# Kernel optimization log

Measured on AMD Instinct MI355X. Metric: run time of the kernel, lower is better.

## Reference

```python
import jax, jax.numpy as jnp
import numpy as np

INIT_STDEV = 0.01

def setup_inputs() -> dict:
    key = jax.random.key(0)
    k1, k2, k3 = jax.random.split(key, 3)
    B, S, D = 8, 4096, 768
    x = jax.random.normal(k1, (B, S, D), dtype=jnp.float32)
    att_v = jax.random.normal(k2, (D,), dtype=jnp.float32) * INIT_STDEV
    att_W = jax.random.normal(k3, (D, D), dtype=jnp.float32) * INIT_STDEV
    return {"x": x, "att_v": att_v, "att_W": att_W}

def reference(x, att_v, att_W):
    # y = x @ W : [B,S,D]; scores = tanh(y) . v over D : [B,S]
    y = jnp.tanh(jnp.einsum('bsd,de->bse', x, att_W))
    scores = jnp.einsum('bsd,d->bs', y, att_v)
    weights = jax.nn.softmax(scores, axis=-1)            # softmax over sequence
    out = jnp.einsum('bs,bsd->bd', weights, x)           # attsum pool
    return out.astype(jnp.float32)
```

## Files before the change

### kernel.cpp

```cpp
#include <hip/hip_runtime.h>
#include <hip/hip_bf16.h>

constexpr int Bb = 8;
constexpr int Ss = 4096;
constexpr int Dd = 768;
constexpr int Mm = Bb * Ss;

typedef __bf16 bf16x8 __attribute__((ext_vector_type(8)));
typedef __bf16 bf16x4 __attribute__((ext_vector_type(4)));
typedef float f32x4 __attribute__((ext_vector_type(4)));

__device__ __forceinline__ float fast_tanh(float x) {
    return 1.f - 2.f / (__expf(2.f * x) + 1.f);
}

__device__ __forceinline__ void load_lds16(const void* g, void* l) {
    __builtin_amdgcn_global_load_lds(
        (const __attribute__((address_space(1))) unsigned int*)g,
        (__attribute__((address_space(3))) unsigned int*)l, 16, 0, 0);
}

__global__ __launch_bounds__(256) void convW(const float* __restrict__ W,
                                             __bf16* __restrict__ Wt) {
    __shared__ float tile[32][33];
    const int tx = threadIdx.x & 31;
    const int ty = threadIdx.x >> 5;
    const int kb = blockIdx.x * 32;
    const int nb = blockIdx.y * 32;
#pragma unroll
    for (int i = 0; i < 32; i += 8)
        tile[ty + i][tx] = W[(size_t)(kb + ty + i) * Dd + nb + tx];
    __syncthreads();
#pragma unroll
    for (int i = 0; i < 32; i += 8) {
        const int n = nb + ty + i;
        const int txs = (tx & 7) | ((((tx >> 3) & 3) ^ ((n >> 1) & 3)) << 3);
        Wt[(size_t)n * Dd + kb + txs] = (__bf16)tile[tx][ty + i];
    }
}

__global__ __launch_bounds__(512, 4) void scores_gemm(
    const float* __restrict__ x, const __bf16* __restrict__ Wt,
    const float* __restrict__ v, float* __restrict__ scores3) {
    __shared__ __bf16 As[3][128 * 32];
    __shared__ __bf16 Bs[3][256 * 32];
    __shared__ float ssc[8][64];

    const int t = threadIdx.x;
    const int id = blockIdx.x;
    const int ids = ((id & 7) * 96) + (id >> 3);
    const int mb = ids / 3;
    const int nb = ids - mb * 3;
    const int lane = t & 63;
    const int wave = t >> 6;
    const int wm = wave >> 2;
    const int wn = wave & 3;
    const int quad = lane >> 4;
    const int lid = lane & 15;
    const int rslot = ((quad ^ ((lid >> 1) & 3)) * 8);

    const int arow = t >> 2;
    const int aslotraw = t & 3;
    const int aslot = aslotraw ^ ((arow >> 1) & 3);
    const float* agp = x + (size_t)(mb * 128 + arow) * Dd + aslotraw * 8;
    const int awr = arow * 32 + aslot * 8;

    const __bf16* bg[2];
    int bl[2];
#pragma unroll
    for (int j = 0; j < 2; ++j) {
        const int flat = j * 8192 + t * 16;
        const int col = flat >> 6;
        bg[j] = Wt + (size_t)(nb * 256 + col) * Dd + ((flat & 63) >> 1);
        bl[j] = flat >> 1;
    }

    f32x4 acc[4][4];
#pragma unroll
    for (int tm = 0; tm < 4; ++tm)
#pragma unroll
        for (int nt = 0; nt < 4; ++nt) acc[tm][nt] = (f32x4){0.f, 0.f, 0.f, 0.f};

    {
        const float4 pa0 = *(const float4*)(agp);
        const float4 pa1 = *(const float4*)(agp + 4);
#pragma unroll
        for (int j = 0; j < 2; ++j) load_lds16(bg[j], &Bs[0][bl[j]]);
#pragma unroll
        for (int j = 0; j < 2; ++j) load_lds16(bg[j] + 32, &Bs[1][bl[j]]);
        bf16x8 w;
        w[0] = (__bf16)pa0.x; w[1] = (__bf16)pa0.y; w[2] = (__bf16)pa0.z; w[3] = (__bf16)pa0.w;
        w[4] = (__bf16)pa1.x; w[5] = (__bf16)pa1.y; w[6] = (__bf16)pa1.z; w[7] = (__bf16)pa1.w;
        *(bf16x8*)(&As[0][awr]) = w;
    }

#pragma unroll
    for (int k = 0; k < 24; ++k) {
        if (k == 23) asm volatile("s_waitcnt vmcnt(0) lgkmcnt(0)" ::: "memory");
        else         asm volatile("s_waitcnt vmcnt(2) lgkmcnt(0)" ::: "memory");
        __builtin_amdgcn_sched_barrier(0);
        __builtin_amdgcn_s_barrier();
        __builtin_amdgcn_sched_barrier(0);

        float4 a0n, a1n;
        if (k < 23) {
            a0n = *(const float4*)(agp + (k + 1) * 32);
            a1n = *(const float4*)(agp + (k + 1) * 32 + 4);
        }
        __builtin_amdgcn_sched_barrier(0);
        if (k < 22) {
#pragma unroll
            for (int j = 0; j < 2; ++j)
                load_lds16(bg[j] + (k + 2) * 32, &Bs[(k + 2) % 3][bl[j]]);
        }

        bf16x8 af[4], bfr[4];
#pragma unroll
        for (int tm = 0; tm < 4; ++tm)
            af[tm] = *(const bf16x8*)(&As[k % 3][(wm * 64 + tm * 16 + lid) * 32 + rslot]);
#pragma unroll
        for (int nt = 0; nt < 4; ++nt)
            bfr[nt] = *(const bf16x8*)(&Bs[k % 3][(wn * 64 + nt * 16 + lid) * 32 + rslot]);

        __builtin_amdgcn_s_setprio(1);
#pragma unroll
        for (int tm = 0; tm < 4; ++tm)
#pragma unroll
            for (int nt = 0; nt < 4; ++nt)
                acc[tm][nt] = __builtin_amdgcn_mfma_f32_16x16x32_bf16(af[tm], bfr[nt], acc[tm][nt], 0, 0, 0);
        __builtin_amdgcn_s_setprio(0);

        if (k < 23) {
            bf16x8 pa;
            pa[0] = (__bf16)a0n.x; pa[1] = (__bf16)a0n.y; pa[2] = (__bf16)a0n.z; pa[3] = (__bf16)a0n.w;
            pa[4] = (__bf16)a1n.x; pa[5] = (__bf16)a1n.y; pa[6] = (__bf16)a1n.z; pa[7] = (__bf16)a1n.w;
            *(bf16x8*)(&As[(k + 1) % 3][awr]) = pa;
        }
    }

    float vv[4];
#pragma unroll
    for (int nt = 0; nt < 4; ++nt)
        vv[nt] = v[nb * 256 + wn * 64 + nt * 16 + lid];

#pragma unroll
    for (int tm = 0; tm < 4; ++tm)
#pragma unroll
        for (int r = 0; r < 4; ++r) {
            float s = 0.f;
#pragma unroll
            for (int nt = 0; nt < 4; ++nt) s += vv[nt] * fast_tanh(acc[tm][nt][r]);
            s += __shfl_xor(s, 1);
            s += __shfl_xor(s, 2);
            s += __shfl_xor(s, 4);
            s += __shfl_xor(s, 8);
            if (lid == 0) ssc[wave][tm * 16 + quad * 4 + r] = s;
        }
    __syncthreads();
    if (t < 128) {
        const int wmh = t >> 6;
        const int rl = t & 63;
        float s = 0.f;
#pragma unroll
        for (int ww = 0; ww < 4; ++ww) s += ssc[wmh * 4 + ww][rl];
        scores3[(size_t)nb * Mm + mb * 128 + t] = s;
    }
}

__global__ __launch_bounds__(256) void softmax_k(const float* __restrict__ scores3,
                                                 float* __restrict__ weights,
                                                 float* __restrict__ sinv) {
    const int b = blockIdx.x;
    const int t = threadIdx.x;
    const float* s0 = scores3 + (size_t)b * Ss;
    const float* s1 = s0 + Mm;
    const float* s2 = s1 + Mm;
    float* wgt = weights + (size_t)b * Ss;
    __shared__ float red[256];

    float mx = -1e30f;
    for (int i = t; i < Ss; i += 256) {
        const float sc = s0[i] + s1[i] + s2[i];
        wgt[i] = sc;
        mx = fmaxf(mx, sc);
    }
    red[t] = mx;
    __syncthreads();
    for (int o = 128; o > 0; o >>= 1) {
        if (t < o) red[t] = fmaxf(red[t], red[t + o]);
        __syncthreads();
    }
    mx = red[0];
    __syncthreads();
    float sum = 0.f;
    for (int i = t; i < Ss; i += 256) {
        const float e = __expf(wgt[i] - mx);
        wgt[i] = e;
        sum += e;
    }
    red[t] = sum;
    __syncthreads();
    for (int o = 128; o > 0; o >>= 1) {
        if (t < o) red[t] += red[t + o];
        __syncthreads();
    }
    if (t == 0) sinv[b] = 1.f / red[0];
}

__global__ __launch_bounds__(192) void pool1(const float* __restrict__ x,
                                             const float* __restrict__ weights,
                                             const float* __restrict__ sinv,
                                             float* __restrict__ out) {
    const int b = blockIdx.y;
    const int c = blockIdx.x;
    const int t = threadIdx.x;
    const float* base = x + ((size_t)b * Ss + c * 32) * Dd;
    const float* wrow = weights + (size_t)b * Ss + c * 32;
    float4 acc = make_float4(0.f, 0.f, 0.f, 0.f);
#pragma unroll 8
    for (int i = 0; i < 32; ++i) {
        const float ww = wrow[i];
        const float4 xv = *(const float4*)(base + (size_t)i * Dd + t * 4);
        acc.x += ww * xv.x;
        acc.y += ww * xv.y;
        acc.z += ww * xv.z;
        acc.w += ww * xv.w;
    }
    const float inv = sinv[b];
    float* o = out + (size_t)b * Dd + t * 4;
    atomicAdd(o + 0, acc.x * inv);
    atomicAdd(o + 1, acc.y * inv);
    atomicAdd(o + 2, acc.z * inv);
    atomicAdd(o + 3, acc.w * inv);
}

extern "C" void kernel_launch(void* const* d_in, const int* in_sizes, int n_in,
                              void* d_out, int out_size, void* d_ws, size_t ws_size,
                              hipStream_t stream) {
    (void)in_sizes; (void)n_in; (void)ws_size; (void)out_size;
    const float* x = (const float*)d_in[0];
    const float* v = (const float*)d_in[1];
    const float* W = (const float*)d_in[2];

    char* ws = (char*)d_ws;
    __bf16* Wt = (__bf16*)ws;
    float* scores3 = (float*)(ws + 1179648);
    float* weights = (float*)(ws + 1179648 + 393216);
    float* sinv    = (float*)(ws + 1179648 + 393216 + 131072);

    hipMemsetAsync(d_out, 0, Bb * Dd * sizeof(float), stream);

    convW<<<dim3(Dd / 32, Dd / 32), 256, 0, stream>>>(W, Wt);
    scores_gemm<<<dim3(3 * Mm / 128), 512, 0, stream>>>(x, Wt, v, scores3);
    softmax_k<<<dim3(Bb), 256, 0, stream>>>(scores3, weights, sinv);
    pool1<<<dim3(128, Bb), 192, 0, stream>>>(x, weights, sinv, (float*)d_out);
}
```

Measured before the change: 242.7 us.

## Stream fp32 A tiles to LDS via direct loads; replace atomics with two-pass reduction

```diff
diff --git a/kernel.cpp b/kernel.cpp
--- a/kernel.cpp
+++ b/kernel.cpp
@@ -7,7 +7,6 @@
 constexpr int Mm = Bb * Ss;
 
 typedef __bf16 bf16x8 __attribute__((ext_vector_type(8)));
-typedef __bf16 bf16x4 __attribute__((ext_vector_type(4)));
 typedef float f32x4 __attribute__((ext_vector_type(4)));
 
 __device__ __forceinline__ float fast_tanh(float x) {
@@ -42,9 +41,8 @@
 __global__ __launch_bounds__(512, 4) void scores_gemm(
     const float* __restrict__ x, const __bf16* __restrict__ Wt,
     const float* __restrict__ v, float* __restrict__ scores3) {
-    __shared__ __bf16 As[3][128 * 32];
+    __shared__ float  As[2][128 * 32];
     __shared__ __bf16 Bs[3][256 * 32];
-    __shared__ float ssc[8][64];
 
     const int t = threadIdx.x;
     const int id = blockIdx.x;
@@ -59,21 +57,35 @@
     const int lid = lane & 15;
     const int rslot = ((quad ^ ((lid >> 1) & 3)) * 8);
 
-    const int arow = t >> 2;
-    const int aslotraw = t & 3;
-    const int aslot = aslotraw ^ ((arow >> 1) & 3);
-    const float* agp = x + (size_t)(mb * 128 + arow) * Dd + aslotraw * 8;
-    const int awr = arow * 32 + aslot * 8;
-
-    const __bf16* bg[2];
-    int bl[2];
+    const int sarow = t >> 3;
+    const int sarot = ((sarow & 1) << 2) | ((sarow >> 1) & 3);
+    const int sacoll = (t & 7) ^ sarot;
+    const float* axp = x + (size_t)(mb * 128 + sarow) * Dd + sacoll * 4;
+    const float* axp1 = axp + (size_t)64 * Dd;
+
+    const __bf16* bg[3];
+    int bl[3];
+#pragma unroll
+    for (int j = 0; j < 3; ++j) {
+        const int flat = j * 8192 / 3 * 3;
+        (void)flat;
+        const int f2 = j * 8192 + t * 16;
+        (void)f2;
+        bg[j] = nullptr; bl[j] = 0;
+    }
+    const __bf16* bgp[2];
+    int blp[2];
 #pragma unroll
     for (int j = 0; j < 2; ++j) {
         const int flat = j * 8192 + t * 16;
         const int col = flat >> 6;
-        bg[j] = Wt + (size_t)(nb * 256 + col) * Dd + ((flat & 63) >> 1);
-        bl[j] = flat >> 1;
-    }
+        bgp[j] = Wt + (size_t)(nb * 256 + col) * Dd + ((flat & 63) >> 1);
+        blp[j] = flat >> 1;
+    }
+
+    const int arot = ((lid & 1) << 2) | ((lid >> 1) & 3);
+    const int s0 = ((2 * quad) ^ arot) * 4;
+    const int s1 = ((2 * quad + 1) ^ arot) * 4;
 
     f32x4 acc[4][4];
 #pragma unroll
@@ -81,43 +93,45 @@
 #pragma unroll
         for (int nt = 0; nt < 4; ++nt) acc[tm][nt] = (f32x4){0.f, 0.f, 0.f, 0.f};
 
-    {
-        const float4 pa0 = *(const float4*)(agp);
-        const float4 pa1 = *(const float4*)(agp + 4);
-#pragma unroll
-        for (int j = 0; j < 2; ++j) load_lds16(bg[j], &Bs[0][bl[j]]);
-#pragma unroll
-        for (int j = 0; j < 2; ++j) load_lds16(bg[j] + 32, &Bs[1][bl[j]]);
-        bf16x8 w;
-        w[0] = (__bf16)pa0.x; w[1] = (__bf16)pa0.y; w[2] = (__bf16)pa0.z; w[3] = (__bf16)pa0.w;
-        w[4] = (__bf16)pa1.x; w[5] = (__bf16)pa1.y; w[6] = (__bf16)pa1.z; w[7] = (__bf16)pa1.w;
-        *(bf16x8*)(&As[0][awr]) = w;
-    }
+    load_lds16(axp, &As[0][t * 4]);
+    load_lds16(axp1, &As[0][2048 + t * 4]);
+#pragma unroll
+    for (int j = 0; j < 2; ++j) load_lds16(bgp[j], &Bs[0][blp[j]]);
+#pragma unroll
+    for (int j = 0; j < 2; ++j) load_lds16(bgp[j] + 32, &Bs[1][blp[j]]);
 
 #pragma unroll
     for (int k = 0; k < 24; ++k) {
-        if (k == 23) asm volatile("s_waitcnt vmcnt(0) lgkmcnt(0)" ::: "memory");
-        else         asm volatile("s_waitcnt vmcnt(2) lgkmcnt(0)" ::: "memory");
+        if (k == 23) asm volatile("s_waitcnt vmcnt(0)" ::: "memory");
+        else         asm volatile("s_waitcnt vmcnt(2)" ::: "memory");
         __builtin_amdgcn_sched_barrier(0);
         __builtin_amdgcn_s_barrier();
         __builtin_amdgcn_sched_barrier(0);
 
-        float4 a0n, a1n;
         if (k < 23) {
-            a0n = *(const float4*)(agp + (k + 1) * 32);
-            a1n = *(const float4*)(agp + (k + 1) * 32 + 4);
+            load_lds16(axp + (k + 1) * 32, &As[(k + 1) & 1][t * 4]);
+            load_lds16(axp1 + (k + 1) * 32, &As[(k + 1) & 1][2048 + t * 4]);
+        }
+        if (k < 22) {
+#pragma unroll
+            for (int j = 0; j < 2; ++j)
+                load_lds16(bgp[j] + (k + 2) * 32, &Bs[(k + 2) % 3][blp[j]]);
         }
         __builtin_amdgcn_sched_barrier(0);
-        if (k < 22) {
-#pragma unroll
-            for (int j = 0; j < 2; ++j)
-                load_lds16(bg[j] + (k + 2) * 32, &Bs[(k + 2) % 3][bl[j]]);
-        }
 
         bf16x8 af[4], bfr[4];
 #pragma unroll
-        for (int tm = 0; tm < 4; ++tm)
-            af[tm] = *(const bf16x8*)(&As[k % 3][(wm * 64 + tm * 16 + lid) * 32 + rslot]);
+        for (int tm = 0; tm < 4; ++tm) {
+            const int rowb = (wm * 64 + tm * 16 + lid) * 32;
+            const f32x4 lo = *(const f32x4*)(&As[k & 1][rowb + s0]);
+            const f32x4 hi = *(const f32x4*)(&As[k & 1][rowb + s1]);
+            bf16x8 a;
+            a[0] = (__bf16)lo[0]; a[1] = (__bf16)lo[1];
+            a[2] = (__bf16)lo[2]; a[3] = (__bf16)lo[3];
+            a[4] = (__bf16)hi[0]; a[5] = (__bf16)hi[1];
+            a[6] = (__bf16)hi[2]; a[7] = (__bf16)hi[3];
+            af[tm] = a;
+        }
 #pragma unroll
         for (int nt = 0; nt < 4; ++nt)
             bfr[nt] = *(const bf16x8*)(&Bs[k % 3][(wn * 64 + nt * 16 + lid) * 32 + rslot]);
@@ -129,14 +143,10 @@
             for (int nt = 0; nt < 4; ++nt)
                 acc[tm][nt] = __builtin_amdgcn_mfma_f32_16x16x32_bf16(af[tm], bfr[nt], acc[tm][nt], 0, 0, 0);
         __builtin_amdgcn_s_setprio(0);
-
-        if (k < 23) {
-            bf16x8 pa;
-            pa[0] = (__bf16)a0n.x; pa[1] = (__bf16)a0n.y; pa[2] = (__bf16)a0n.z; pa[3] = (__bf16)a0n.w;
-            pa[4] = (__bf16)a1n.x; pa[5] = (__bf16)a1n.y; pa[6] = (__bf16)a1n.z; pa[7] = (__bf16)a1n.w;
-            *(bf16x8*)(&As[(k + 1) % 3][awr]) = pa;
-        }
-    }
+    }
+
+    __syncthreads();
+    float* ssc = (float*)&As[0][0];
 
     float vv[4];
 #pragma unroll
@@ -154,7 +164,7 @@
             s += __shfl_xor(s, 2);
             s += __shfl_xor(s, 4);
             s += __shfl_xor(s, 8);
-            if (lid == 0) ssc[wave][tm * 16 + quad * 4 + r] = s;
+            if (lid == 0) ssc[wave * 64 + tm * 16 + quad * 4 + r] = s;
         }
     __syncthreads();
     if (t < 128) {
@@ -162,7 +172,7 @@
         const int rl = t & 63;
         float s = 0.f;
 #pragma unroll
-        for (int ww = 0; ww < 4; ++ww) s += ssc[wmh * 4 + ww][rl];
+        for (int ww = 0; ww < 4; ++ww) s += ssc[(wmh * 4 + ww) * 64 + rl];
         scores3[(size_t)nb * Mm + mb * 128 + t] = s;
     }
 }
@@ -209,8 +219,7 @@
 
 __global__ __launch_bounds__(192) void pool1(const float* __restrict__ x,
                                              const float* __restrict__ weights,
-                                             const float* __restrict__ sinv,
-                                             float* __restrict__ out) {
+                                             float* __restrict__ partial) {
     const int b = blockIdx.y;
     const int c = blockIdx.x;
     const int t = threadIdx.x;
@@ -226,12 +235,18 @@
         acc.z += ww * xv.z;
         acc.w += ww * xv.w;
     }
-    const float inv = sinv[b];
-    float* o = out + (size_t)b * Dd + t * 4;
-    atomicAdd(o + 0, acc.x * inv);
-    atomicAdd(o + 1, acc.y * inv);
-    atomicAdd(o + 2, acc.z * inv);
-    atomicAdd(o + 3, acc.w * inv);
+    *(float4*)(partial + ((size_t)(b * 128 + c)) * Dd + t * 4) = acc;
+}
+
+__global__ __launch_bounds__(768) void pool2(const float* __restrict__ partial,
+                                             const float* __restrict__ sinv,
+                                             float* __restrict__ out) {
+    const int b = blockIdx.x;
+    const int d = threadIdx.x;
+    float s = 0.f;
+#pragma unroll 8
+    for (int c = 0; c < 128; ++c) s += partial[((size_t)(b * 128 + c)) * Dd + d];
+    out[(size_t)b * Dd + d] = s * sinv[b];
 }
 
 extern "C" void kernel_launch(void* const* d_in, const int* in_sizes, int n_in,
@@ -247,11 +262,11 @@
     float* scores3 = (float*)(ws + 1179648);
     float* weights = (float*)(ws + 1179648 + 393216);
     float* sinv    = (float*)(ws + 1179648 + 393216 + 131072);
-
-    hipMemsetAsync(d_out, 0, Bb * Dd * sizeof(float), stream);
+    float* partial = (float*)(ws + 1179648 + 393216 + 131072 + 32);
 
     convW<<<dim3(Dd / 32, Dd / 32), 256, 0, stream>>>(W, Wt);
     scores_gemm<<<dim3(3 * Mm / 128), 512, 0, stream>>>(x, Wt, v, scores3);
     softmax_k<<<dim3(Bb), 256, 0, stream>>>(scores3, weights, sinv);
-    pool1<<<dim3(128, Bb), 192, 0, stream>>>(x, weights, sinv, (float*)d_out);
-}
+    pool1<<<dim3(128, Bb), 192, 0, stream>>>(x, weights, partial);
+    pool2<<<dim3(Bb), 768, 0, stream>>>(partial, sinv, (float*)d_out);
+}
```

Measured after the change: 245.7 us. Within noise of the previous version (+1.2%).
